# Kernel optimization log

Hardware: AMD Instinct MI355X
Metric: run time of the kernel (lower is better)

The kernel has to match this reference:

```python
import jax, jax.numpy as jnp
import numpy as np

B, NPER, F, D, E, NUM_STEPS = 256, 512, 256, 32, 524288, 4
N = B * NPER
INIT_TAU, TAU_SCALE, STEP_ALPHA = 0.1, 0.5, 5.0


def setup_inputs() -> dict:
    key = jax.random.key(0)
    ks = jax.random.split(key, 10)
    x_start = jax.random.uniform(ks[0], (N,), jnp.float32, 0.1, 1.0)   # strictly positive iterate
    x_solution = jax.random.uniform(ks[1], (N,), jnp.float32, 0.0, 1.0)
    q = jax.random.normal(ks[2], (N,), jnp.float32)
    edge_src = jax.random.randint(ks[3], (E,), 0, N, jnp.int32)
    edge_dst = jax.random.randint(ks[4], (E,), 0, N, jnp.int32)
    vals_batch = jnp.repeat(jnp.arange(B, dtype=jnp.int32), NPER)      # equal-sized graphs
    proj_matrix = jax.random.normal(ks[5], (B, NPER, F), jnp.float32) / np.float32(np.sqrt(NPER))
    W_in = jax.random.normal(ks[6], (2, D), jnp.float32) / np.float32(np.sqrt(2.0))
    b_in = jnp.zeros((D,), jnp.float32)
    W_msg = jax.random.normal(ks[7], (D, D), jnp.float32) / np.float32(np.sqrt(D))
    b_msg = jnp.zeros((D,), jnp.float32)
    W_out = jax.random.normal(ks[8], (D, 1), jnp.float32) / np.float32(np.sqrt(D))
    b_out = jnp.zeros((1,), jnp.float32)
    return {"x_start": x_start, "x_solution": x_solution, "q": q,
            "proj_matrix": proj_matrix, "W_in": W_in, "b_in": b_in,
            "W_msg": W_msg, "b_msg": b_msg, "W_out": W_out, "b_out": b_out,
            "edge_src": edge_src, "edge_dst": edge_dst, "vals_batch": vals_batch}


def _l1_normalize(x, batch):
    # per-graph L1 normalization: x / sum_i |x_i| over the graph segment
    s = jax.ops.segment_sum(jnp.abs(x), batch, num_segments=B)
    return x / (s[batch] + 1e-12)


def _line_search(x, d, batch, max_alpha):
    # largest per-graph alpha s.t. x + alpha*d >= 0, capped at max_alpha
    ratio = jnp.where(d < 0, x / jnp.maximum(-d, 1e-12), max_alpha)
    a = jnp.clip(jax.ops.segment_min(ratio, batch, num_segments=B), 0.0, max_alpha)
    return a[batch]  # gathered back to per-node


def _gnn(xs, q, edge_src, edge_dst, W_in, b_in, W_msg, b_msg, W_out, b_out):
    h = jax.nn.relu(jnp.stack([xs, q], axis=-1) @ W_in + b_in)      # [N, D]
    m = h[edge_src] @ W_msg + b_msg                                  # [E, D]
    agg = jax.ops.segment_sum(m, edge_dst, num_segments=N)          # [N, D]
    h2 = jax.nn.relu(h + agg)
    return h2 @ W_out[:, 0] + b_out[0]                               # [N]


def reference(x_start, x_solution, q, proj_matrix, W_in, b_in, W_msg, b_msg,
              W_out, b_out, edge_src, edge_dst, vals_batch):
    tau = INIT_TAU
    xs = x_start
    preds, labels = [], []
    for _ in range(NUM_STEPS):
        pred = _gnn(xs, q, edge_src, edge_dst, W_in, b_in, W_msg, b_msg, W_out, b_out)
        preds.append(pred)
        labels.append(_l1_normalize(x_solution - xs, vals_batch))
        p = _l1_normalize(jax.lax.stop_gradient(pred), vals_batch)   # .detach() in torch
        direction = p + 3.0 * tau / (xs + tau)
        tau = max(tau * TAU_SCALE, 1e-5)
        # to_dense_batch with equal graph sizes == reshape; project onto nullspace basis
        dd = direction.reshape(B, NPER)
        df = jnp.einsum('bnf,bn->bf', proj_matrix, dd)               # [B, F]
        pproj = jnp.einsum('bnf,bf->bn', proj_matrix, df).reshape(-1)  # [N]
        alpha = _line_search(xs, pproj, vals_batch, STEP_ALPHA) * 0.995
        xs = xs + alpha * pproj
    return jnp.stack(preds, axis=1), jnp.stack(labels, axis=1)       # each [N, NUM_STEPS]
```

## Files before the change

### kernel.cpp

```cpp
#include <hip/hip_runtime.h>

#define BB 256
#define NPER 512
#define FF 256
#define DD 32
#define EE 524288
#define NN (BB*NPER)
#define NSTEPS 4

__device__ __forceinline__ float bflo(unsigned u) { return __uint_as_float(u << 16); }
__device__ __forceinline__ float bfhi(unsigned u) { return __uint_as_float(u & 0xFFFF0000u); }
__device__ __forceinline__ unsigned rtn_bf16(unsigned u) {
    return (u + 0x7FFFu + ((u >> 16) & 1u)) >> 16;
}


__global__ void k_degpack(const int* __restrict__ dst, unsigned* __restrict__ deg,
                          const float* __restrict__ xs0, const float* __restrict__ q,
                          float2* __restrict__ xq) {
    int t = blockIdx.x * blockDim.x + threadIdx.x;
    if (t < NN) { float2 v; v.x = xs0[t]; v.y = q[t]; xq[t] = v; }
    atomicAdd(&deg[dst[t]], 1u);
}

__global__ void k_bsum(const unsigned* __restrict__ deg, unsigned* __restrict__ bsum) {
    __shared__ unsigned r[256];
    int t = threadIdx.x;
    r[t] = deg[blockIdx.x * 256 + t];
    __syncthreads();
    for (int o = 128; o > 0; o >>= 1) { if (t < o) r[t] += r[t + o]; __syncthreads(); }
    if (t == 0) bsum[blockIdx.x] = r[0];
}

__global__ void k_scanb(const unsigned* __restrict__ bsum, unsigned* __restrict__ bbase) {
    __shared__ unsigned r[512];
    int t = threadIdx.x;
    unsigned own = bsum[t];
    r[t] = own;
    __syncthreads();
    for (int o = 1; o < 512; o <<= 1) {
        unsigned v = (t >= o) ? r[t - o] : 0u;
        __syncthreads();
        r[t] += v;
        __syncthreads();
    }
    bbase[t] = r[t] - own;
}

__global__ void k_offsets(const unsigned* __restrict__ deg, const unsigned* __restrict__ bbase,
                          unsigned* __restrict__ rowstart, unsigned* __restrict__ cursor) {
    __shared__ unsigned r[256];
    int t = threadIdx.x;
    int i = blockIdx.x * 256 + t;
    unsigned d = deg[i];
    r[t] = d;
    __syncthreads();
    for (int o = 1; o < 256; o <<= 1) {
        unsigned v = (t >= o) ? r[t - o] : 0u;
        __syncthreads();
        r[t] += v;
        __syncthreads();
    }
    unsigned excl = r[t] - d + bbase[blockIdx.x];
    rowstart[i] = excl;
    cursor[i] = excl;
}

__global__ void k_fill(const int* __restrict__ src, const int* __restrict__ dst,
                       unsigned* __restrict__ cursor, int* __restrict__ csr_src) {
    int e = blockIdx.x * blockDim.x + threadIdx.x;
    unsigned pos = atomicAdd(&cursor[dst[e]], 1u);
    csr_src[pos] = src[e];
}


__global__ void k_node_g(const float2* __restrict__ xq,
                         const float* __restrict__ Win, const float* __restrict__ bin,
                         const unsigned* __restrict__ rowstart, const unsigned* __restrict__ deg,
                         const int* __restrict__ csr_src,
                         const float* __restrict__ Wmsg, const float* __restrict__ bmsg,
                         const float* __restrict__ Wout, const float* __restrict__ bout,
                         float* __restrict__ pred, float* __restrict__ out_preds, int step) {
    int tid = threadIdx.x;
    int d = tid & 31;
    int i = blockIdx.x * 8 + (tid >> 5);
    float w0 = Win[d], w1 = Win[DD + d], b0 = bin[d];
    float wcol[DD];
    #pragma unroll
    for (int k = 0; k < DD; ++k) wcol[k] = Wmsg[k * DD + d];
    unsigned rs = rowstart[i];
    unsigned dg = deg[i];
    unsigned nfull = dg < 32u ? dg : 32u;
    float xv = 0.f, qv = 0.f;
    if ((unsigned)d < nfull) {
        int sv = csr_src[rs + d];
        float2 v = xq[sv];
        xv = v.x; qv = v.y;
    }
    float s = 0.f;
    for (unsigned j = 0; j < nfull; ++j) {
        float xj = __shfl(xv, (int)j, 32);
        float qj = __shfl(qv, (int)j, 32);
        s += fmaxf(xj * w0 + qj * w1 + b0, 0.f);
    }
    for (unsigned j = 32; j < dg; ++j) {
        int sv = csr_src[rs + j];
        float2 v = xq[sv];
        s += fmaxf(v.x * w0 + v.y * w1 + b0, 0.f);
    }
    float2 self = xq[i];
    float hval = fmaxf(self.x * w0 + self.y * w1 + b0, 0.f);
    float agg = (float)dg * bmsg[d];
    #pragma unroll
    for (int k = 0; k < DD; ++k) agg += __shfl(s, k, 32) * wcol[k];
    float h2 = fmaxf(hval + agg, 0.f);
    float v = h2 * Wout[d];
    for (int o = 16; o > 0; o >>= 1) v += __shfl_down(v, o, 32);
    if (d == 0) {
        float pr = v + bout[0];
        pred[i] = pr;
        out_preds[i * NSTEPS + step] = pr;
    }
}

__global__ __launch_bounds__(1024) void k_step(const float* __restrict__ Pf,
                                               unsigned short* __restrict__ Pbf,
                                               float2* __restrict__ xq,
                                               const float* __restrict__ xsol,
                                               const float* __restrict__ pred,
                                               float* __restrict__ out_labels,
                                               float tau, int step) {
    __shared__ float ddl[NPER];
    __shared__ float sl[16 * FF];
    __shared__ float dfl[FF];
    __shared__ float pp[NPER];
    __shared__ float red[16], red2[16];
    int b = blockIdx.x;
    int t = threadIdx.x;
    int w = t >> 6, lane = t & 63;
    int i = b * NPER + (t & (NPER - 1));
    float x = 0.f, r = 0.f, p = 0.f;
    float a1 = 0.f, a2 = 0.f;
    if (t < NPER) {
        x = xq[i].x;
        r = xsol[i] - x;
        p = pred[i];
        a1 = fabsf(r); a2 = fabsf(p);
    }
    #pragma unroll
    for (int o = 32; o > 0; o >>= 1) {
        a1 += __shfl_down(a1, o, 64);
        a2 += __shfl_down(a2, o, 64);
    }
    if (lane == 0) { red[w] = a1; red2[w] = a2; }
    __syncthreads();
    float Sr = 1e-12f, Sp = 1e-12f;
    #pragma unroll
    for (int k = 0; k < 8; ++k) { Sr += red[k]; Sp += red2[k]; }
    if (t < NPER) out_labels[i * NSTEPS + step] = r / Sr;
    if (step == NSTEPS - 1) return;
    if (t < NPER) ddl[t] = p / Sp + 3.0f * tau / (x + tau);
    __syncthreads();

    float4 acc = {0.f, 0.f, 0.f, 0.f};
    size_t rowbase = (size_t)(b * NPER + w * 32) * FF;
    const float* dw = &ddl[w * 32];
    if (step == 0) {
        const float4* Pr = (const float4*)(Pf + rowbase) + lane;
        uint2* Pw = (uint2*)(Pbf + rowbase) + lane;
        #pragma unroll 4
        for (int n = 0; n < 32; ++n) {
            float4 pv = Pr[(size_t)n * 64];
            float sc = dw[n];
            acc.x += pv.x * sc; acc.y += pv.y * sc;
            acc.z += pv.z * sc; acc.w += pv.w * sc;
            unsigned u0 = rtn_bf16(__float_as_uint(pv.x));
            unsigned u1 = rtn_bf16(__float_as_uint(pv.y));
            unsigned u2 = rtn_bf16(__float_as_uint(pv.z));
            unsigned u3 = rtn_bf16(__float_as_uint(pv.w));
            uint2 o; o.x = u0 | (u1 << 16); o.y = u2 | (u3 << 16);
            Pw[(size_t)n * 64] = o;
        }
    } else {
        const uint2* Pr = (const uint2*)(Pbf + rowbase) + lane;
        #pragma unroll 8
        for (int n = 0; n < 32; ++n) {
            uint2 pv = Pr[(size_t)n * 64];
            float sc = dw[n];
            acc.x += bflo(pv.x) * sc; acc.y += bfhi(pv.x) * sc;
            acc.z += bflo(pv.y) * sc; acc.w += bfhi(pv.y) * sc;
        }
    }
    ((float4*)sl)[w * 64 + lane] = acc;
    __syncthreads();
    if (t < FF) {
        float v = 0.f;
        #pragma unroll
        for (int k = 0; k < 16; ++k) v += sl[k * FF + t];
        dfl[t] = v;
    }
    __syncthreads();

    int g = t >> 5, l5 = t & 31;
    float4 dfa = ((const float4*)dfl)[l5 * 2];
    float4 dfb = ((const float4*)dfl)[l5 * 2 + 1];
    const uint4* Pr4 = (const uint4*)(Pbf + (size_t)(b * NPER + g * 16) * FF) + l5;
    #pragma unroll 4
    for (int it = 0; it < 16; ++it) {
        uint4 pv = Pr4[(size_t)it * 32];
        float a = bflo(pv.x) * dfa.x + bfhi(pv.x) * dfa.y
                + bflo(pv.y) * dfa.z + bfhi(pv.y) * dfa.w
                + bflo(pv.z) * dfb.x + bfhi(pv.z) * dfb.y
                + bflo(pv.w) * dfb.z + bfhi(pv.w) * dfb.w;
        #pragma unroll
        for (int o = 16; o > 0; o >>= 1) a += __shfl_down(a, o, 32);
        if (l5 == 0) pp[g * 16 + it] = a;
    }
    __syncthreads();

    float d = 0.f, m = 5.0f;
    if (t < NPER) {
        d = pp[t];
        m = (d < 0.f) ? (x / fmaxf(-d, 1e-12f)) : 5.0f;
    }
    #pragma unroll
    for (int o = 32; o > 0; o >>= 1) m = fminf(m, __shfl_down(m, o, 64));
    if (lane == 0) red[w] = m;
    __syncthreads();
    float mm = red[0];
    #pragma unroll
    for (int k = 1; k < 16; ++k) mm = fminf(mm, red[k]);
    float alpha = fminf(fmaxf(mm, 0.f), 5.0f) * 0.995f;
    if (t < NPER) xq[i].x = x + alpha * d;
}


extern "C" void kernel_launch(void* const* d_in, const int* in_sizes, int n_in,
                              void* d_out, int out_size, void* d_ws, size_t ws_size,
                              hipStream_t stream) {
    const float* x_start = (const float*)d_in[0];
    const float* x_sol   = (const float*)d_in[1];
    const float* q       = (const float*)d_in[2];
    const float* P       = (const float*)d_in[3];
    const float* Win     = (const float*)d_in[4];
    const float* bin     = (const float*)d_in[5];
    const float* Wmsg    = (const float*)d_in[6];
    const float* bmsg    = (const float*)d_in[7];
    const float* Wout    = (const float*)d_in[8];
    const float* bout    = (const float*)d_in[9];
    const int*   esrc    = (const int*)d_in[10];
    const int*   edst    = (const int*)d_in[11];

    float* out_preds  = (float*)d_out;
    float* out_labels = (float*)d_out + (size_t)NN * NSTEPS;

    float* w = (float*)d_ws;
    float2* xq  = (float2*)w; w += 2 * (size_t)NN;
    float* pred  = w; w += NN;
    unsigned* deg      = (unsigned*)w; w += NN;
    unsigned* rowstart = (unsigned*)w; w += NN;
    unsigned* cursor   = (unsigned*)w; w += NN;
    unsigned* bsum     = (unsigned*)w; w += NN / 256;
    unsigned* bbase    = (unsigned*)w; w += NN / 256;
    int* csr_src       = (int*)w;      w += EE;
    unsigned short* Pbf = (unsigned short*)w;

    hipMemsetAsync(deg, 0, NN * sizeof(unsigned), stream);
    k_degpack<<<EE / 256, 256, 0, stream>>>(edst, deg, x_start, q, xq);
    k_bsum<<<NN / 256, 256, 0, stream>>>(deg, bsum);
    k_scanb<<<1, NN / 256, 0, stream>>>(bsum, bbase);
    k_offsets<<<NN / 256, 256, 0, stream>>>(deg, bbase, rowstart, cursor);
    k_fill<<<EE / 256, 256, 0, stream>>>(esrc, edst, cursor, csr_src);

    float tau = 0.1f;
    for (int step = 0; step < NSTEPS; ++step) {
        k_node_g<<<NN / 8, 256, 0, stream>>>(xq, Win, bin, rowstart, deg, csr_src,
                                             Wmsg, bmsg, Wout, bout, pred, out_preds, step);
        k_step<<<BB, 1024, 0, stream>>>(P, Pbf, xq, x_sol, pred, out_labels, tau, step);
        tau = fmaxf(tau * 0.5f, 1e-5f);
    }
}
```

Baseline: 504.7 us.

## Split per-graph step kernel into multi-kernel pipeline with more blocks

The monolithic per-graph k_step kernel (256 blocks of 1024 threads) is replaced by four kernels: label/direction computation, a projection reduction split across 8 blocks per graph with atomic accumulation into df, a back-projection kernel with one row per 32-lane group, and a line-search/update kernel. This spreads the 128MB fp32 / 64MB bf16 projection-matrix streaming over far more blocks so more of the GPU's CUs are used. In exchange it adds extra launches per step, global round-trips for dd/df/pp, and float atomics that make the summation order nondeterministic.

```diff
diff --git a/kernel.cpp b/kernel.cpp
--- a/kernel.cpp
+++ b/kernel.cpp
@@ -123,115 +123,143 @@
     }
 }
 
-__global__ __launch_bounds__(1024) void k_step(const float* __restrict__ Pf,
-                                               unsigned short* __restrict__ Pbf,
-                                               float2* __restrict__ xq,
-                                               const float* __restrict__ xsol,
-                                               const float* __restrict__ pred,
-                                               float* __restrict__ out_labels,
-                                               float tau, int step) {
-    __shared__ float ddl[NPER];
-    __shared__ float sl[16 * FF];
-    __shared__ float dfl[FF];
-    __shared__ float pp[NPER];
-    __shared__ float red[16], red2[16];
+__global__ __launch_bounds__(512) void k_dd(const float2* __restrict__ xq,
+                                            const float* __restrict__ xsol,
+                                            const float* __restrict__ pred,
+                                            float* __restrict__ out_labels,
+                                            float* __restrict__ dd,
+                                            float* __restrict__ df,
+                                            float tau, int step) {
     int b = blockIdx.x;
     int t = threadIdx.x;
     int w = t >> 6, lane = t & 63;
-    int i = b * NPER + (t & (NPER - 1));
-    float x = 0.f, r = 0.f, p = 0.f;
-    float a1 = 0.f, a2 = 0.f;
-    if (t < NPER) {
-        x = xq[i].x;
-        r = xsol[i] - x;
-        p = pred[i];
-        a1 = fabsf(r); a2 = fabsf(p);
-    }
+    int i = b * NPER + t;
+    float x = xq[i].x;
+    float r = xsol[i] - x;
+    float p = pred[i];
+    float a1 = fabsf(r), a2 = fabsf(p);
     #pragma unroll
     for (int o = 32; o > 0; o >>= 1) {
         a1 += __shfl_down(a1, o, 64);
         a2 += __shfl_down(a2, o, 64);
     }
+    __shared__ float red[8], red2[8];
     if (lane == 0) { red[w] = a1; red2[w] = a2; }
     __syncthreads();
     float Sr = 1e-12f, Sp = 1e-12f;
     #pragma unroll
     for (int k = 0; k < 8; ++k) { Sr += red[k]; Sp += red2[k]; }
-    if (t < NPER) out_labels[i * NSTEPS + step] = r / Sr;
+    out_labels[i * NSTEPS + step] = r / Sr;
     if (step == NSTEPS - 1) return;
-    if (t < NPER) ddl[t] = p / Sp + 3.0f * tau / (x + tau);
-    __syncthreads();
-
+    dd[i] = p / Sp + 3.0f * tau / (x + tau);
+    if (t < FF) df[b * FF + t] = 0.f;
+}
+
+__global__ __launch_bounds__(256) void k_df0(const float* __restrict__ Pf,
+                                             unsigned short* __restrict__ Pbf,
+                                             const float* __restrict__ dd,
+                                             float* __restrict__ df) {
+    int blk = blockIdx.x;
+    int b = blk >> 3, s = blk & 7;
+    int t = threadIdx.x;
+    int w = t >> 6, lane = t & 63;
+    int row0 = s * 64 + w * 16;
+    const float* ddp = dd + b * NPER + row0;
+    size_t base = (size_t)(b * NPER + row0) * FF;
+    const float4* Pr = (const float4*)(Pf + base) + lane;
+    uint2* Pw = (uint2*)(Pbf + base) + lane;
     float4 acc = {0.f, 0.f, 0.f, 0.f};
-    size_t rowbase = (size_t)(b * NPER + w * 32) * FF;
-    const float* dw = &ddl[w * 32];
-    if (step == 0) {
-        const float4* Pr = (const float4*)(Pf + rowbase) + lane;
-        uint2* Pw = (uint2*)(Pbf + rowbase) + lane;
-        #pragma unroll 4
-        for (int n = 0; n < 32; ++n) {
-            float4 pv = Pr[(size_t)n * 64];
-            float sc = dw[n];
-            acc.x += pv.x * sc; acc.y += pv.y * sc;
-            acc.z += pv.z * sc; acc.w += pv.w * sc;
-            unsigned u0 = rtn_bf16(__float_as_uint(pv.x));
-            unsigned u1 = rtn_bf16(__float_as_uint(pv.y));
-            unsigned u2 = rtn_bf16(__float_as_uint(pv.z));
-            unsigned u3 = rtn_bf16(__float_as_uint(pv.w));
-            uint2 o; o.x = u0 | (u1 << 16); o.y = u2 | (u3 << 16);
-            Pw[(size_t)n * 64] = o;
-        }
-    } else {
-        const uint2* Pr = (const uint2*)(Pbf + rowbase) + lane;
-        #pragma unroll 8
-        for (int n = 0; n < 32; ++n) {
-            uint2 pv = Pr[(size_t)n * 64];
-            float sc = dw[n];
-            acc.x += bflo(pv.x) * sc; acc.y += bfhi(pv.x) * sc;
-            acc.z += bflo(pv.y) * sc; acc.w += bfhi(pv.y) * sc;
-        }
-    }
+    #pragma unroll 4
+    for (int n = 0; n < 16; ++n) {
+        float4 pv = Pr[(size_t)n * 64];
+        float sc = ddp[n];
+        acc.x += pv.x * sc; acc.y += pv.y * sc;
+        acc.z += pv.z * sc; acc.w += pv.w * sc;
+        unsigned u0 = rtn_bf16(__float_as_uint(pv.x));
+        unsigned u1 = rtn_bf16(__float_as_uint(pv.y));
+        unsigned u2 = rtn_bf16(__float_as_uint(pv.z));
+        unsigned u3 = rtn_bf16(__float_as_uint(pv.w));
+        uint2 o; o.x = u0 | (u1 << 16); o.y = u2 | (u3 << 16);
+        Pw[(size_t)n * 64] = o;
+    }
+    __shared__ float sl[4 * FF];
     ((float4*)sl)[w * 64 + lane] = acc;
     __syncthreads();
     if (t < FF) {
-        float v = 0.f;
-        #pragma unroll
-        for (int k = 0; k < 16; ++k) v += sl[k * FF + t];
-        dfl[t] = v;
-    }
-    __syncthreads();
-
+        float v = sl[t] + sl[FF + t] + sl[2 * FF + t] + sl[3 * FF + t];
+        atomicAdd(&df[b * FF + t], v);
+    }
+}
+
+__global__ __launch_bounds__(256) void k_dfb(const unsigned short* __restrict__ Pbf,
+                                             const float* __restrict__ dd,
+                                             float* __restrict__ df) {
+    int blk = blockIdx.x;
+    int b = blk >> 3, s = blk & 7;
+    int t = threadIdx.x;
+    int w = t >> 6, lane = t & 63;
+    int row0 = s * 64 + w * 16;
+    const float* ddp = dd + b * NPER + row0;
+    size_t base = (size_t)(b * NPER + row0) * FF;
+    const uint2* Pr = (const uint2*)(Pbf + base) + lane;
+    float4 acc = {0.f, 0.f, 0.f, 0.f};
+    #pragma unroll 8
+    for (int n = 0; n < 16; ++n) {
+        uint2 pv = Pr[(size_t)n * 64];
+        float sc = ddp[n];
+        acc.x += bflo(pv.x) * sc; acc.y += bfhi(pv.x) * sc;
+        acc.z += bflo(pv.y) * sc; acc.w += bfhi(pv.y) * sc;
+    }
+    __shared__ float sl[4 * FF];
+    ((float4*)sl)[w * 64 + lane] = acc;
+    __syncthreads();
+    if (t < FF) {
+        float v = sl[t] + sl[FF + t] + sl[2 * FF + t] + sl[3 * FF + t];
+        atomicAdd(&df[b * FF + t], v);
+    }
+}
+
+__global__ __launch_bounds__(256) void k_pp(const unsigned short* __restrict__ Pbf,
+                                            const float* __restrict__ df,
+                                            float* __restrict__ pp) {
+    int t = threadIdx.x;
     int g = t >> 5, l5 = t & 31;
+    int i = blockIdx.x * 8 + g;
+    int b = i >> 9;
+    __shared__ float dfl[FF];
+    if (t < FF) dfl[t] = df[b * FF + t];
+    __syncthreads();
     float4 dfa = ((const float4*)dfl)[l5 * 2];
-    float4 dfb = ((const float4*)dfl)[l5 * 2 + 1];
-    const uint4* Pr4 = (const uint4*)(Pbf + (size_t)(b * NPER + g * 16) * FF) + l5;
-    #pragma unroll 4
-    for (int it = 0; it < 16; ++it) {
-        uint4 pv = Pr4[(size_t)it * 32];
-        float a = bflo(pv.x) * dfa.x + bfhi(pv.x) * dfa.y
-                + bflo(pv.y) * dfa.z + bfhi(pv.y) * dfa.w
-                + bflo(pv.z) * dfb.x + bfhi(pv.z) * dfb.y
-                + bflo(pv.w) * dfb.z + bfhi(pv.w) * dfb.w;
-        #pragma unroll
-        for (int o = 16; o > 0; o >>= 1) a += __shfl_down(a, o, 32);
-        if (l5 == 0) pp[g * 16 + it] = a;
-    }
-    __syncthreads();
-
-    float d = 0.f, m = 5.0f;
-    if (t < NPER) {
-        d = pp[t];
-        m = (d < 0.f) ? (x / fmaxf(-d, 1e-12f)) : 5.0f;
-    }
+    float4 dfb4 = ((const float4*)dfl)[l5 * 2 + 1];
+    uint4 pv = *((const uint4*)(Pbf + (size_t)i * FF) + l5);
+    float a = bflo(pv.x) * dfa.x + bfhi(pv.x) * dfa.y
+            + bflo(pv.y) * dfa.z + bfhi(pv.y) * dfa.w
+            + bflo(pv.z) * dfb4.x + bfhi(pv.z) * dfb4.y
+            + bflo(pv.w) * dfb4.z + bfhi(pv.w) * dfb4.w;
+    #pragma unroll
+    for (int o = 16; o > 0; o >>= 1) a += __shfl_down(a, o, 32);
+    if (l5 == 0) pp[i] = a;
+}
+
+__global__ __launch_bounds__(512) void k_upd(const float* __restrict__ pp,
+                                             float2* __restrict__ xq) {
+    int b = blockIdx.x;
+    int t = threadIdx.x;
+    int w = t >> 6, lane = t & 63;
+    int i = b * NPER + t;
+    float x = xq[i].x;
+    float d = pp[i];
+    float m = (d < 0.f) ? (x / fmaxf(-d, 1e-12f)) : 5.0f;
     #pragma unroll
     for (int o = 32; o > 0; o >>= 1) m = fminf(m, __shfl_down(m, o, 64));
+    __shared__ float red[8];
     if (lane == 0) red[w] = m;
     __syncthreads();
     float mm = red[0];
     #pragma unroll
-    for (int k = 1; k < 16; ++k) mm = fminf(mm, red[k]);
+    for (int k = 1; k < 8; ++k) mm = fminf(mm, red[k]);
     float alpha = fminf(fmaxf(mm, 0.f), 5.0f) * 0.995f;
-    if (t < NPER) xq[i].x = x + alpha * d;
+    xq[i].x = x + alpha * d;
 }
 
 
@@ -257,6 +285,9 @@
     float* w = (float*)d_ws;
     float2* xq  = (float2*)w; w += 2 * (size_t)NN;
     float* pred  = w; w += NN;
+    float* dd    = w; w += NN;
+    float* df    = w; w += (size_t)BB * FF;
+    float* pp    = w; w += NN;
     unsigned* deg      = (unsigned*)w; w += NN;
     unsigned* rowstart = (unsigned*)w; w += NN;
     unsigned* cursor   = (unsigned*)w; w += NN;
@@ -276,7 +307,13 @@
     for (int step = 0; step < NSTEPS; ++step) {
         k_node_g<<<NN / 8, 256, 0, stream>>>(xq, Win, bin, rowstart, deg, csr_src,
                                              Wmsg, bmsg, Wout, bout, pred, out_preds, step);
-        k_step<<<BB, 1024, 0, stream>>>(P, Pbf, xq, x_sol, pred, out_labels, tau, step);
+        k_dd<<<BB, 512, 0, stream>>>(xq, x_sol, pred, out_labels, dd, df, tau, step);
+        if (step < NSTEPS - 1) {
+            if (step == 0) k_df0<<<BB * 8, 256, 0, stream>>>(P, Pbf, dd, df);
+            else           k_dfb<<<BB * 8, 256, 0, stream>>>(Pbf, dd, df);
+            k_pp<<<NN / 8, 256, 0, stream>>>(Pbf, df, pp);
+            k_upd<<<BB, 512, 0, stream>>>(pp, xq);
+        }
         tau = fmaxf(tau * 0.5f, 1e-5f);
     }
 }
```

Result: no change. 511.8 us (+1.4%).

## Keep bf16 projection tile in registers across both matvecs and fuse line search

Applied to the files above, without the earlier changes.

The fp32-to-bf16 cast of the projection matrix moves out of the first step into its own grid-wide kernel. Each warp's 32-row bf16 slice of P is now loaded once into registers and reused for both the P^T·d and P·df products, so P is read once per step instead of twice. The per-row projection results feed the line-search minimum directly in the same loop. The last step uses a small labels-only kernel. The cost is 64 extra registers per thread at 1024-thread blocks, plus a full-wavefront xor reduction per row in place of the earlier 32-lane reductions.

```diff
diff --git a/kernel.cpp b/kernel.cpp
--- a/kernel.cpp
+++ b/kernel.cpp
@@ -71,6 +71,19 @@
     int e = blockIdx.x * blockDim.x + threadIdx.x;
     unsigned pos = atomicAdd(&cursor[dst[e]], 1u);
     csr_src[pos] = src[e];
+}
+
+__global__ __launch_bounds__(256) void k_cast(const float* __restrict__ Pf,
+                                              unsigned short* __restrict__ Pbf) {
+    size_t idx = ((size_t)blockIdx.x * 256 + threadIdx.x) * 8;
+    float4 a = *(const float4*)(Pf + idx);
+    float4 c = *(const float4*)(Pf + idx + 4);
+    uint4 o;
+    o.x = rtn_bf16(__float_as_uint(a.x)) | (rtn_bf16(__float_as_uint(a.y)) << 16);
+    o.y = rtn_bf16(__float_as_uint(a.z)) | (rtn_bf16(__float_as_uint(a.w)) << 16);
+    o.z = rtn_bf16(__float_as_uint(c.x)) | (rtn_bf16(__float_as_uint(c.y)) << 16);
+    o.w = rtn_bf16(__float_as_uint(c.z)) | (rtn_bf16(__float_as_uint(c.w)) << 16);
+    *(uint4*)(Pbf + idx) = o;
 }
 
 
@@ -123,28 +136,26 @@
     }
 }
 
-__global__ __launch_bounds__(1024) void k_step(const float* __restrict__ Pf,
-                                               unsigned short* __restrict__ Pbf,
+__global__ __launch_bounds__(1024) void k_proj(const unsigned short* __restrict__ Pbf,
                                                float2* __restrict__ xq,
                                                const float* __restrict__ xsol,
                                                const float* __restrict__ pred,
                                                float* __restrict__ out_labels,
                                                float tau, int step) {
-    __shared__ float ddl[NPER];
+    __shared__ float dd_l[NPER], x_l[NPER], pp_l[NPER];
     __shared__ float sl[16 * FF];
     __shared__ float dfl[FF];
-    __shared__ float pp[NPER];
-    __shared__ float red[16], red2[16];
+    __shared__ float redA[16], redB[16], wmin[16];
     int b = blockIdx.x;
     int t = threadIdx.x;
     int w = t >> 6, lane = t & 63;
-    int i = b * NPER + (t & (NPER - 1));
-    float x = 0.f, r = 0.f, p = 0.f;
-    float a1 = 0.f, a2 = 0.f;
+    int gbase = b * NPER;
+
+    float x = 0.f, r = 0.f, p = 0.f, a1 = 0.f, a2 = 0.f;
     if (t < NPER) {
-        x = xq[i].x;
-        r = xsol[i] - x;
-        p = pred[i];
+        x = xq[gbase + t].x;
+        r = xsol[gbase + t] - x;
+        p = pred[gbase + t];
         a1 = fabsf(r); a2 = fabsf(p);
     }
     #pragma unroll
@@ -152,44 +163,34 @@
         a1 += __shfl_down(a1, o, 64);
         a2 += __shfl_down(a2, o, 64);
     }
-    if (lane == 0) { red[w] = a1; red2[w] = a2; }
+    if (lane == 0) { redA[w] = a1; redB[w] = a2; }
     __syncthreads();
     float Sr = 1e-12f, Sp = 1e-12f;
     #pragma unroll
-    for (int k = 0; k < 8; ++k) { Sr += red[k]; Sp += red2[k]; }
-    if (t < NPER) out_labels[i * NSTEPS + step] = r / Sr;
-    if (step == NSTEPS - 1) return;
-    if (t < NPER) ddl[t] = p / Sp + 3.0f * tau / (x + tau);
-    __syncthreads();
-
+    for (int k = 0; k < 16; ++k) { Sr += redA[k]; Sp += redB[k]; }
+    if (t < NPER) {
+        out_labels[(size_t)(gbase + t) * NSTEPS + step] = r / Sr;
+        x_l[t] = x;
+        dd_l[t] = p / Sp + 3.0f * tau / (x + tau);
+    }
+    __syncthreads();
+
+    size_t pbase = ((size_t)(gbase + w * 32)) * FF + 4 * lane;
+    const uint2* Pr = (const uint2*)(Pbf + pbase);
+    unsigned pl[64];
+    #pragma unroll
+    for (int n = 0; n < 32; ++n) {
+        uint2 pv = Pr[(size_t)n * 64];
+        pl[2 * n] = pv.x; pl[2 * n + 1] = pv.y;
+    }
     float4 acc = {0.f, 0.f, 0.f, 0.f};
-    size_t rowbase = (size_t)(b * NPER + w * 32) * FF;
-    const float* dw = &ddl[w * 32];
-    if (step == 0) {
-        const float4* Pr = (const float4*)(Pf + rowbase) + lane;
-        uint2* Pw = (uint2*)(Pbf + rowbase) + lane;
-        #pragma unroll 4
-        for (int n = 0; n < 32; ++n) {
-            float4 pv = Pr[(size_t)n * 64];
-            float sc = dw[n];
-            acc.x += pv.x * sc; acc.y += pv.y * sc;
-            acc.z += pv.z * sc; acc.w += pv.w * sc;
-            unsigned u0 = rtn_bf16(__float_as_uint(pv.x));
-            unsigned u1 = rtn_bf16(__float_as_uint(pv.y));
-            unsigned u2 = rtn_bf16(__float_as_uint(pv.z));
-            unsigned u3 = rtn_bf16(__float_as_uint(pv.w));
-            uint2 o; o.x = u0 | (u1 << 16); o.y = u2 | (u3 << 16);
-            Pw[(size_t)n * 64] = o;
-        }
-    } else {
-        const uint2* Pr = (const uint2*)(Pbf + rowbase) + lane;
-        #pragma unroll 8
-        for (int n = 0; n < 32; ++n) {
-            uint2 pv = Pr[(size_t)n * 64];
-            float sc = dw[n];
-            acc.x += bflo(pv.x) * sc; acc.y += bfhi(pv.x) * sc;
-            acc.z += bflo(pv.y) * sc; acc.w += bfhi(pv.y) * sc;
-        }
+    #pragma unroll
+    for (int n = 0; n < 32; ++n) {
+        float sc = dd_l[w * 32 + n];
+        acc.x += bflo(pl[2 * n]) * sc;
+        acc.y += bfhi(pl[2 * n]) * sc;
+        acc.z += bflo(pl[2 * n + 1]) * sc;
+        acc.w += bfhi(pl[2 * n + 1]) * sc;
     }
     ((float4*)sl)[w * 64 + lane] = acc;
     __syncthreads();
@@ -201,37 +202,48 @@
     }
     __syncthreads();
 
-    int g = t >> 5, l5 = t & 31;
-    float4 dfa = ((const float4*)dfl)[l5 * 2];
-    float4 dfb = ((const float4*)dfl)[l5 * 2 + 1];
-    const uint4* Pr4 = (const uint4*)(Pbf + (size_t)(b * NPER + g * 16) * FF) + l5;
-    #pragma unroll 4
-    for (int it = 0; it < 16; ++it) {
-        uint4 pv = Pr4[(size_t)it * 32];
-        float a = bflo(pv.x) * dfa.x + bfhi(pv.x) * dfa.y
-                + bflo(pv.y) * dfa.z + bfhi(pv.y) * dfa.w
-                + bflo(pv.z) * dfb.x + bfhi(pv.z) * dfb.y
-                + bflo(pv.w) * dfb.z + bfhi(pv.w) * dfb.w;
+    float4 dfv = ((const float4*)dfl)[lane];
+    float mloc = 5.0f;
+    #pragma unroll
+    for (int n = 0; n < 32; ++n) {
+        float pr = bflo(pl[2 * n]) * dfv.x + bfhi(pl[2 * n]) * dfv.y
+                 + bflo(pl[2 * n + 1]) * dfv.z + bfhi(pl[2 * n + 1]) * dfv.w;
         #pragma unroll
-        for (int o = 16; o > 0; o >>= 1) a += __shfl_down(a, o, 32);
-        if (l5 == 0) pp[g * 16 + it] = a;
-    }
-    __syncthreads();
-
-    float d = 0.f, m = 5.0f;
-    if (t < NPER) {
-        d = pp[t];
-        m = (d < 0.f) ? (x / fmaxf(-d, 1e-12f)) : 5.0f;
-    }
-    #pragma unroll
-    for (int o = 32; o > 0; o >>= 1) m = fminf(m, __shfl_down(m, o, 64));
-    if (lane == 0) red[w] = m;
-    __syncthreads();
-    float mm = red[0];
-    #pragma unroll
-    for (int k = 1; k < 16; ++k) mm = fminf(mm, red[k]);
+        for (int o = 1; o < 64; o <<= 1) pr += __shfl_xor(pr, o, 64);
+        if (lane == 0) pp_l[w * 32 + n] = pr;
+        float xr = x_l[w * 32 + n];
+        float ratio = (pr < 0.f) ? (xr / fmaxf(-pr, 1e-12f)) : 5.0f;
+        mloc = fminf(mloc, ratio);
+    }
+    if (lane == 0) wmin[w] = mloc;
+    __syncthreads();
+
+    float mm = wmin[0];
+    #pragma unroll
+    for (int k = 1; k < 16; ++k) mm = fminf(mm, wmin[k]);
     float alpha = fminf(fmaxf(mm, 0.f), 5.0f) * 0.995f;
-    if (t < NPER) xq[i].x = x + alpha * d;
+    if (t < NPER) xq[gbase + t].x = x_l[t] + alpha * pp_l[t];
+}
+
+__global__ __launch_bounds__(512) void k_lab(const float2* __restrict__ xq,
+                                             const float* __restrict__ xsol,
+                                             float* __restrict__ out_labels, int step) {
+    int b = blockIdx.x;
+    int t = threadIdx.x;
+    int w = t >> 6, lane = t & 63;
+    int i = b * NPER + t;
+    float x = xq[i].x;
+    float r = xsol[i] - x;
+    float a1 = fabsf(r);
+    #pragma unroll
+    for (int o = 32; o > 0; o >>= 1) a1 += __shfl_down(a1, o, 64);
+    __shared__ float red[8];
+    if (lane == 0) red[w] = a1;
+    __syncthreads();
+    float Sr = 1e-12f;
+    #pragma unroll
+    for (int k = 0; k < 8; ++k) Sr += red[k];
+    out_labels[(size_t)i * NSTEPS + step] = r / Sr;
 }
 
 
@@ -267,6 +279,7 @@
 
     hipMemsetAsync(deg, 0, NN * sizeof(unsigned), stream);
     k_degpack<<<EE / 256, 256, 0, stream>>>(edst, deg, x_start, q, xq);
+    k_cast<<<(NN / 256) * (FF / 8), 256, 0, stream>>>(P, Pbf);
     k_bsum<<<NN / 256, 256, 0, stream>>>(deg, bsum);
     k_scanb<<<1, NN / 256, 0, stream>>>(bsum, bbase);
     k_offsets<<<NN / 256, 256, 0, stream>>>(deg, bbase, rowstart, cursor);
@@ -276,7 +289,11 @@
     for (int step = 0; step < NSTEPS; ++step) {
         k_node_g<<<NN / 8, 256, 0, stream>>>(xq, Win, bin, rowstart, deg, csr_src,
                                              Wmsg, bmsg, Wout, bout, pred, out_preds, step);
-        k_step<<<BB, 1024, 0, stream>>>(P, Pbf, xq, x_sol, pred, out_labels, tau, step);
+        if (step < NSTEPS - 1) {
+            k_proj<<<BB, 1024, 0, stream>>>(Pbf, xq, x_sol, pred, out_labels, tau, step);
+        } else {
+            k_lab<<<BB, 512, 0, stream>>>(xq, x_sol, out_labels, step);
+        }
         tau = fmaxf(tau * 0.5f, 1e-5f);
     }
 }
```

Result: slower. 544.4 us (+7.9%).
